# Performance work log

Measured on AMD Instinct MI355X. Metric: run time of the kernel, lower is better.

Reference implementation:

```python
import jax, jax.numpy as jnp
import numpy as np

LAYER_SIZE = [784, 128, 64, 10]
ACTIVE_FUN = ["relu", "relu", "linear"]
BATCH = 65536


def setup_inputs() -> dict:
    key = jax.random.key(0)
    k_x, k0, k1, k2 = jax.random.split(key, 4)
    X = jax.random.normal(k_x, (BATCH, LAYER_SIZE[0]), dtype=jnp.float32)
    # weights mimic torch init: 0.1 * rand(in+1, out)
    W0 = 0.1 * jax.random.uniform(k0, (LAYER_SIZE[0] + 1, LAYER_SIZE[1]), dtype=jnp.float32)
    W1 = 0.1 * jax.random.uniform(k1, (LAYER_SIZE[1] + 1, LAYER_SIZE[2]), dtype=jnp.float32)
    W2 = 0.1 * jax.random.uniform(k2, (LAYER_SIZE[2] + 1, LAYER_SIZE[3]), dtype=jnp.float32)
    return {"X": X, "W0": W0, "W1": W1, "W2": W2}


def _act(h, name):
    if name == "sigmoid":
        return jax.nn.sigmoid(h)
    if name == "relu":
        return jnp.maximum(h, 0.0)
    if name == "tanh":
        return jnp.tanh(h)
    return h  # linear


def _mlp(X, weights):
    h = X
    for W, act in zip(weights, ACTIVE_FUN):
        # bias folded in: concat a column of ones (original concats scalar 1 per sample)
        ones = jnp.ones((h.shape[0], 1), dtype=h.dtype)
        h = jnp.concatenate([h, ones], axis=1) @ W
        h = _act(h, act)
    return h


def reference(X, W0, W1, W2):
    # Batched equivalent of the per-sample Python loop: returns [B, 10] predictions
    return _mlp(X, [W0, W1, W2])
```

## Files before the change

kernel.cpp:

```cpp
#include <hip/hip_runtime.h>

typedef unsigned short u16;
typedef __attribute__((ext_vector_type(4))) float f32x4;
typedef __attribute__((ext_vector_type(8))) short short8;

#define D0 784
#define D1 128
#define D2 64
#define D3 10
#define KS0 25
#define KS1 4
#define KS2 2

#define WS_W0P 0
#define WS_W1P 204800
#define WS_W2P 221184
#define WS_B0  223232
#define WS_B1  223744
#define WS_B2  224000

__device__ __forceinline__ u16 f2bf(float f) {
  union { float f; unsigned u; } v; v.f = f;
  unsigned u = v.u;
  return (u16)((u + 0x7fffu + ((u >> 16) & 1u)) >> 16);
}

__device__ __forceinline__ int swz(int c, int kk) {
  return c * 32 + (((kk >> 3) ^ ((c >> 1) & 3)) << 3) + (kk & 7);
}

__global__ void prep_kernel(const float* __restrict__ W0, const float* __restrict__ W1,
                            const float* __restrict__ W2, u16* __restrict__ w0p,
                            u16* __restrict__ w1p, u16* __restrict__ w2p,
                            float* __restrict__ b0, float* __restrict__ b1,
                            float* __restrict__ b2) {
  int idx = blockIdx.x * 256 + threadIdx.x;
  if (idx < 25 * 128 * 32) {
    int ks = idx / 4096, rem = idx % 4096, c = rem >> 5, kk = rem & 31;
    int k = ks * 32 + kk;
    float v = (k < D0) ? W0[k * D1 + c] : 0.f;
    w0p[ks * 4096 + swz(c, kk)] = f2bf(v);
    return;
  }
  idx -= 25 * 128 * 32;
  if (idx < 4 * 64 * 32) {
    int ks = idx / 2048, rem = idx % 2048, c = rem >> 5, kk = rem & 31;
    int k = ks * 32 + kk;
    w1p[ks * 2048 + swz(c, kk)] = f2bf(W1[k * D2 + c]);
    return;
  }
  idx -= 4 * 64 * 32;
  if (idx < 2 * 16 * 32) {
    int ks = idx / 512, rem = idx % 512, c = rem >> 5, kk = rem & 31;
    int k = ks * 32 + kk;
    float v = (c < D3) ? W2[k * D3 + c] : 0.f;
    w2p[ks * 512 + swz(c, kk)] = f2bf(v);
    return;
  }
  idx -= 2 * 16 * 32;
  if (idx < 128) { b0[idx] = W0[D0 * D1 + idx]; return; }
  idx -= 128;
  if (idx < 64) { b1[idx] = W1[D1 * D2 + idx]; return; }
  idx -= 64;
  if (idx < 16) { b2[idx] = (idx < D3) ? W2[D2 * D3 + idx] : 0.f; }
}

__device__ __forceinline__ void gload_lds16(const void* g, void* l) {
  __builtin_amdgcn_global_load_lds((const __attribute__((address_space(1))) void*)g,
                                   (__attribute__((address_space(3))) void*)l, 16, 0, 0);
}

__device__ __forceinline__ void cvtpk(unsigned& d, float lo, float hi) {
  asm("v_cvt_pk_bf16_f32 %0, %1, %2" : "=v"(d) : "v"(lo), "v"(hi));
}

__global__ __launch_bounds__(256, 4) void mlp_fused(
    const float* __restrict__ X, const u16* __restrict__ w0p,
    const u16* __restrict__ w1p, const float* __restrict__ b0,
    const float* __restrict__ b1, const float* __restrict__ b2,
    float* __restrict__ out) {
  __shared__ __attribute__((aligned(16))) u16 smW0[2][4096];
  __shared__ __attribute__((aligned(16))) u16 smW12[9216];

  const int t = threadIdx.x;
  const int lane = t & 63;
  const int wv = t >> 6;
  const int q = lane >> 4;
  const int lr = lane & 15;

  {
    const char* src = (const char*)w1p;
    char* dst = (char*)smW12;
    for (int off = wv * 1024; off < 18432; off += 4096)
      gload_lds16(src + off + lane * 16, dst + off);
  }
  auto stageW0 = [&](int buf, int ks) {
    const char* src = (const char*)(w0p + ks * 4096) + wv * 2048 + lane * 16;
    char* dst = (char*)&smW0[buf][0] + wv * 2048;
    gload_lds16(src, dst);
    gload_lds16(src + 1024, dst + 1024);
  };

  const int row = blockIdx.x * 64 + wv * 16 + lr;
  const float* xrow = X + (size_t)row * D0;

  f32x4 acc0[8];
#pragma unroll
  for (int f = 0; f < 8; ++f) acc0[f] = (f32x4){0.f, 0.f, 0.f, 0.f};

  f32x4 xa, xb;
  {
    const f32x4* xp = (const f32x4*)(xrow + q * 8);
    xa = xp[0]; xb = xp[1];
  }
  stageW0(0, 0);
  __syncthreads();

  const int boff = lr * 32 + (q ^ ((lr >> 1) & 3)) * 8;

  int buf = 0;
  for (int ks = 0; ks < KS0; ++ks) {
    if (ks + 1 < KS0) stageW0(buf ^ 1, ks + 1);
    f32x4 na = (f32x4){0.f, 0.f, 0.f, 0.f}, nb = (f32x4){0.f, 0.f, 0.f, 0.f};
    if (ks + 1 < KS0) {
      int kb = (ks + 1) * 32 + q * 8;
      if (kb < D0) {
        const f32x4* xp = (const f32x4*)(xrow + kb);
        na = xp[0]; nb = xp[1];
      }
    }
    union { short8 s; unsigned u[4]; } a;
    cvtpk(a.u[0], xa[0], xa[1]);
    cvtpk(a.u[1], xa[2], xa[3]);
    cvtpk(a.u[2], xb[0], xb[1]);
    cvtpk(a.u[3], xb[2], xb[3]);
    const u16* smb = &smW0[buf][0];
#pragma unroll
    for (int f = 0; f < 8; ++f) {
      short8 b = *(const short8*)(smb + f * 512 + boff);
      acc0[f] = __builtin_amdgcn_mfma_f32_16x16x32_bf16(a.s, b, acc0[f], 0, 0, 0);
    }
    __syncthreads();
    xa = na; xb = nb; buf ^= 1;
  }

  char* hbase = (char*)&smW0[0][0] + wv * 4096;

#pragma unroll
  for (int f = 0; f < 8; ++f) {
    int c = f * 16 + lr;
    float bb = b0[c];
    int chb = ((c >> 3) << 4);
    int cwb = (c & 7) << 1;
#pragma unroll
    for (int r = 0; r < 4; ++r) {
      int rr = q * 4 + r;
      float v = acc0[f][r] + bb;
      *(u16*)(hbase + rr * 256 + (chb ^ ((rr & 7) << 4)) + cwb) = f2bf(fmaxf(v, 0.f));
    }
  }
  __builtin_amdgcn_wave_barrier();

  f32x4 acc1[4];
#pragma unroll
  for (int f = 0; f < 4; ++f) acc1[f] = (f32x4){0.f, 0.f, 0.f, 0.f};
#pragma unroll
  for (int ks = 0; ks < KS1; ++ks) {
    short8 a = *(const short8*)(hbase + lr * 256 + (((ks * 4 + q) ^ (lr & 7)) << 4));
#pragma unroll
    for (int f = 0; f < 4; ++f) {
      int c = f * 16 + lr;
      int js = q ^ ((c >> 1) & 3);
      short8 b = *(const short8*)(smW12 + ks * 2048 + c * 32 + js * 8);
      acc1[f] = __builtin_amdgcn_mfma_f32_16x16x32_bf16(a, b, acc1[f], 0, 0, 0);
    }
  }
#pragma unroll
  for (int f = 0; f < 4; ++f) {
    int c = f * 16 + lr;
    float bb = b1[c];
    int chb = ((c >> 3) << 4);
    int cwb = (c & 7) << 1;
#pragma unroll
    for (int r = 0; r < 4; ++r) {
      int rr = q * 4 + r;
      *(u16*)(hbase + rr * 128 + (chb ^ ((rr & 7) << 4)) + cwb) =
          f2bf(fmaxf(acc1[f][r] + bb, 0.f));
    }
  }
  __builtin_amdgcn_wave_barrier();

  f32x4 acc2 = (f32x4){0.f, 0.f, 0.f, 0.f};
  const u16* w2sm = smW12 + 8192;
#pragma unroll
  for (int ks = 0; ks < KS2; ++ks) {
    short8 a = *(const short8*)(hbase + lr * 128 + (((ks * 4 + q) ^ (lr & 7)) << 4));
    int js = q ^ ((lr >> 1) & 3);
    short8 b = *(const short8*)(w2sm + ks * 512 + lr * 32 + js * 8);
    acc2 = __builtin_amdgcn_mfma_f32_16x16x32_bf16(a, b, acc2, 0, 0, 0);
  }
  if (lr < D3) {
    float bb = b2[lr];
#pragma unroll
    for (int r = 0; r < 4; ++r) {
      int rowg = blockIdx.x * 64 + wv * 16 + q * 4 + r;
      out[rowg * D3 + lr] = acc2[r] + bb;
    }
  }
}

extern "C" void kernel_launch(void* const* d_in, const int* in_sizes, int n_in,
                              void* d_out, int out_size, void* d_ws, size_t ws_size,
                              hipStream_t stream) {
  const float* X  = (const float*)d_in[0];
  const float* W0 = (const float*)d_in[1];
  const float* W1 = (const float*)d_in[2];
  const float* W2 = (const float*)d_in[3];
  float* out = (float*)d_out;
  char* ws = (char*)d_ws;
  u16* w0p = (u16*)(ws + WS_W0P);
  u16* w1p = (u16*)(ws + WS_W1P);
  u16* w2p = (u16*)(ws + WS_W2P);
  float* b0 = (float*)(ws + WS_B0);
  float* b1 = (float*)(ws + WS_B1);
  float* b2 = (float*)(ws + WS_B2);

  prep_kernel<<<437, 256, 0, stream>>>(W0, W1, W2, w0p, w1p, w2p, b0, b1, b2);
  mlp_fused<<<65536 / 64, 256, 0, stream>>>(X, w0p, w1p, b0, b1, b2, out);
}
```

Measured before the change: 45.22 us.

## Read weights directly from global/L2 and process two row tiles per wave

```diff
diff --git a/kernel.cpp b/kernel.cpp
--- a/kernel.cpp
+++ b/kernel.cpp
@@ -23,10 +23,6 @@
   union { float f; unsigned u; } v; v.f = f;
   unsigned u = v.u;
   return (u16)((u + 0x7fffu + ((u >> 16) & 1u)) >> 16);
-}
-
-__device__ __forceinline__ int swz(int c, int kk) {
-  return c * 32 + (((kk >> 3) ^ ((c >> 1) & 3)) << 3) + (kk & 7);
 }
 
 __global__ void prep_kernel(const float* __restrict__ W0, const float* __restrict__ W1,
@@ -39,14 +35,14 @@
     int ks = idx / 4096, rem = idx % 4096, c = rem >> 5, kk = rem & 31;
     int k = ks * 32 + kk;
     float v = (k < D0) ? W0[k * D1 + c] : 0.f;
-    w0p[ks * 4096 + swz(c, kk)] = f2bf(v);
+    w0p[ks * 4096 + c * 32 + kk] = f2bf(v);
     return;
   }
   idx -= 25 * 128 * 32;
   if (idx < 4 * 64 * 32) {
     int ks = idx / 2048, rem = idx % 2048, c = rem >> 5, kk = rem & 31;
     int k = ks * 32 + kk;
-    w1p[ks * 2048 + swz(c, kk)] = f2bf(W1[k * D2 + c]);
+    w1p[ks * 2048 + c * 32 + kk] = f2bf(W1[k * D2 + c]);
     return;
   }
   idx -= 4 * 64 * 32;
@@ -54,7 +50,7 @@
     int ks = idx / 512, rem = idx % 512, c = rem >> 5, kk = rem & 31;
     int k = ks * 32 + kk;
     float v = (c < D3) ? W2[k * D3 + c] : 0.f;
-    w2p[ks * 512 + swz(c, kk)] = f2bf(v);
+    w2p[ks * 512 + c * 32 + kk] = f2bf(v);
     return;
   }
   idx -= 2 * 16 * 32;
@@ -65,22 +61,16 @@
   if (idx < 16) { b2[idx] = (idx < D3) ? W2[D2 * D3 + idx] : 0.f; }
 }
 
-__device__ __forceinline__ void gload_lds16(const void* g, void* l) {
-  __builtin_amdgcn_global_load_lds((const __attribute__((address_space(1))) void*)g,
-                                   (__attribute__((address_space(3))) void*)l, 16, 0, 0);
-}
-
 __device__ __forceinline__ void cvtpk(unsigned& d, float lo, float hi) {
   asm("v_cvt_pk_bf16_f32 %0, %1, %2" : "=v"(d) : "v"(lo), "v"(hi));
 }
 
-__global__ __launch_bounds__(256, 4) void mlp_fused(
+__global__ __launch_bounds__(256, 2) void mlp_fused(
     const float* __restrict__ X, const u16* __restrict__ w0p,
-    const u16* __restrict__ w1p, const float* __restrict__ b0,
-    const float* __restrict__ b1, const float* __restrict__ b2,
-    float* __restrict__ out) {
-  __shared__ __attribute__((aligned(16))) u16 smW0[2][4096];
-  __shared__ __attribute__((aligned(16))) u16 smW12[9216];
+    const u16* __restrict__ w1p, const u16* __restrict__ w2p,
+    const float* __restrict__ b0, const float* __restrict__ b1,
+    const float* __restrict__ b2, float* __restrict__ out) {
+  __shared__ __attribute__((aligned(16))) u16 smH[4][4096];
 
   const int t = threadIdx.x;
   const int lane = t & 63;
@@ -88,124 +78,139 @@
   const int q = lane >> 4;
   const int lr = lane & 15;
 
+  const int rowbase = blockIdx.x * 128 + wv * 32;
+  const float* xr0 = X + (size_t)(rowbase + lr) * D0;
+  const float* xr1 = xr0 + (size_t)16 * D0;
+  const u16* bp0 = w0p + lr * 32 + q * 8;
+
+  f32x4 acc[2][8];
+#pragma unroll
+  for (int m = 0; m < 2; ++m)
+#pragma unroll
+    for (int f = 0; f < 8; ++f) acc[m][f] = (f32x4){0.f, 0.f, 0.f, 0.f};
+
+#pragma unroll
+  for (int ks = 0; ks < KS0 - 1; ++ks) {
+    const f32x4* xp0 = (const f32x4*)(xr0 + ks * 32 + q * 8);
+    const f32x4* xp1 = (const f32x4*)(xr1 + ks * 32 + q * 8);
+    f32x4 x0a = xp0[0], x0b = xp0[1];
+    f32x4 x1a = xp1[0], x1b = xp1[1];
+    short8 b[8];
+#pragma unroll
+    for (int f = 0; f < 8; ++f)
+      b[f] = *(const short8*)(bp0 + ks * 4096 + f * 512);
+    union { short8 s; unsigned u[4]; } a0, a1;
+    cvtpk(a0.u[0], x0a[0], x0a[1]); cvtpk(a0.u[1], x0a[2], x0a[3]);
+    cvtpk(a0.u[2], x0b[0], x0b[1]); cvtpk(a0.u[3], x0b[2], x0b[3]);
+    cvtpk(a1.u[0], x1a[0], x1a[1]); cvtpk(a1.u[1], x1a[2], x1a[3]);
+    cvtpk(a1.u[2], x1b[0], x1b[1]); cvtpk(a1.u[3], x1b[2], x1b[3]);
+#pragma unroll
+    for (int f = 0; f < 8; ++f) {
+      acc[0][f] = __builtin_amdgcn_mfma_f32_16x16x32_bf16(a0.s, b[f], acc[0][f], 0, 0, 0);
+      acc[1][f] = __builtin_amdgcn_mfma_f32_16x16x32_bf16(a1.s, b[f], acc[1][f], 0, 0, 0);
+    }
+  }
   {
-    const char* src = (const char*)w1p;
-    char* dst = (char*)smW12;
-    for (int off = wv * 1024; off < 18432; off += 4096)
-      gload_lds16(src + off + lane * 16, dst + off);
-  }
-  auto stageW0 = [&](int buf, int ks) {
-    const char* src = (const char*)(w0p + ks * 4096) + wv * 2048 + lane * 16;
-    char* dst = (char*)&smW0[buf][0] + wv * 2048;
-    gload_lds16(src, dst);
-    gload_lds16(src + 1024, dst + 1024);
-  };
-
-  const int row = blockIdx.x * 64 + wv * 16 + lr;
-  const float* xrow = X + (size_t)row * D0;
-
-  f32x4 acc0[8];
-#pragma unroll
-  for (int f = 0; f < 8; ++f) acc0[f] = (f32x4){0.f, 0.f, 0.f, 0.f};
-
-  f32x4 xa, xb;
-  {
-    const f32x4* xp = (const f32x4*)(xrow + q * 8);
-    xa = xp[0]; xb = xp[1];
-  }
-  stageW0(0, 0);
-  __syncthreads();
-
-  const int boff = lr * 32 + (q ^ ((lr >> 1) & 3)) * 8;
-
-  int buf = 0;
-  for (int ks = 0; ks < KS0; ++ks) {
-    if (ks + 1 < KS0) stageW0(buf ^ 1, ks + 1);
-    f32x4 na = (f32x4){0.f, 0.f, 0.f, 0.f}, nb = (f32x4){0.f, 0.f, 0.f, 0.f};
-    if (ks + 1 < KS0) {
-      int kb = (ks + 1) * 32 + q * 8;
-      if (kb < D0) {
-        const f32x4* xp = (const f32x4*)(xrow + kb);
-        na = xp[0]; nb = xp[1];
-      }
-    }
-    union { short8 s; unsigned u[4]; } a;
-    cvtpk(a.u[0], xa[0], xa[1]);
-    cvtpk(a.u[1], xa[2], xa[3]);
-    cvtpk(a.u[2], xb[0], xb[1]);
-    cvtpk(a.u[3], xb[2], xb[3]);
-    const u16* smb = &smW0[buf][0];
+    const int ks = KS0 - 1;
+    f32x4 x0a = (f32x4){0.f, 0.f, 0.f, 0.f}, x0b = x0a, x1a = x0a, x1b = x0a;
+    if (q < 2) {
+      const f32x4* xp0 = (const f32x4*)(xr0 + ks * 32 + q * 8);
+      const f32x4* xp1 = (const f32x4*)(xr1 + ks * 32 + q * 8);
+      x0a = xp0[0]; x0b = xp0[1];
+      x1a = xp1[0]; x1b = xp1[1];
+    }
+    short8 b[8];
+#pragma unroll
+    for (int f = 0; f < 8; ++f)
+      b[f] = *(const short8*)(bp0 + ks * 4096 + f * 512);
+    union { short8 s; unsigned u[4]; } a0, a1;
+    cvtpk(a0.u[0], x0a[0], x0a[1]); cvtpk(a0.u[1], x0a[2], x0a[3]);
+    cvtpk(a0.u[2], x0b[0], x0b[1]); cvtpk(a0.u[3], x0b[2], x0b[3]);
+    cvtpk(a1.u[0], x1a[0], x1a[1]); cvtpk(a1.u[1], x1a[2], x1a[3]);
+    cvtpk(a1.u[2], x1b[0], x1b[1]); cvtpk(a1.u[3], x1b[2], x1b[3]);
 #pragma unroll
     for (int f = 0; f < 8; ++f) {
-      short8 b = *(const short8*)(smb + f * 512 + boff);
-      acc0[f] = __builtin_amdgcn_mfma_f32_16x16x32_bf16(a.s, b, acc0[f], 0, 0, 0);
-    }
-    __syncthreads();
-    xa = na; xb = nb; buf ^= 1;
-  }
-
-  char* hbase = (char*)&smW0[0][0] + wv * 4096;
-
+      acc[0][f] = __builtin_amdgcn_mfma_f32_16x16x32_bf16(a0.s, b[f], acc[0][f], 0, 0, 0);
+      acc[1][f] = __builtin_amdgcn_mfma_f32_16x16x32_bf16(a1.s, b[f], acc[1][f], 0, 0, 0);
+    }
+  }
+
+  char* hbase = (char*)&smH[wv][0];
 #pragma unroll
   for (int f = 0; f < 8; ++f) {
     int c = f * 16 + lr;
     float bb = b0[c];
-    int chb = ((c >> 3) << 4);
+    int chb = (c >> 3) << 4;
     int cwb = (c & 7) << 1;
 #pragma unroll
-    for (int r = 0; r < 4; ++r) {
-      int rr = q * 4 + r;
-      float v = acc0[f][r] + bb;
-      *(u16*)(hbase + rr * 256 + (chb ^ ((rr & 7) << 4)) + cwb) = f2bf(fmaxf(v, 0.f));
-    }
+    for (int m = 0; m < 2; ++m)
+#pragma unroll
+      for (int r = 0; r < 4; ++r) {
+        int rr = m * 16 + q * 4 + r;
+        *(u16*)(hbase + rr * 256 + (chb ^ ((rr & 7) << 4)) + cwb) =
+            f2bf(fmaxf(acc[m][f][r] + bb, 0.f));
+      }
   }
   __builtin_amdgcn_wave_barrier();
 
-  f32x4 acc1[4];
-#pragma unroll
-  for (int f = 0; f < 4; ++f) acc1[f] = (f32x4){0.f, 0.f, 0.f, 0.f};
+  f32x4 acc1[2][4];
+#pragma unroll
+  for (int m = 0; m < 2; ++m)
+#pragma unroll
+    for (int f = 0; f < 4; ++f) acc1[m][f] = (f32x4){0.f, 0.f, 0.f, 0.f};
+  const u16* bp1 = w1p + lr * 32 + q * 8;
 #pragma unroll
   for (int ks = 0; ks < KS1; ++ks) {
-    short8 a = *(const short8*)(hbase + lr * 256 + (((ks * 4 + q) ^ (lr & 7)) << 4));
+    short8 a0 = *(const short8*)(hbase + lr * 256 + (((ks * 4 + q) ^ (lr & 7)) << 4));
+    short8 a1 = *(const short8*)(hbase + (16 + lr) * 256 + (((ks * 4 + q) ^ (lr & 7)) << 4));
+    short8 b[4];
+#pragma unroll
+    for (int f = 0; f < 4; ++f)
+      b[f] = *(const short8*)(bp1 + ks * 2048 + f * 512);
 #pragma unroll
     for (int f = 0; f < 4; ++f) {
-      int c = f * 16 + lr;
-      int js = q ^ ((c >> 1) & 3);
-      short8 b = *(const short8*)(smW12 + ks * 2048 + c * 32 + js * 8);
-      acc1[f] = __builtin_amdgcn_mfma_f32_16x16x32_bf16(a, b, acc1[f], 0, 0, 0);
+      acc1[0][f] = __builtin_amdgcn_mfma_f32_16x16x32_bf16(a0, b[f], acc1[0][f], 0, 0, 0);
+      acc1[1][f] = __builtin_amdgcn_mfma_f32_16x16x32_bf16(a1, b[f], acc1[1][f], 0, 0, 0);
     }
   }
 #pragma unroll
   for (int f = 0; f < 4; ++f) {
     int c = f * 16 + lr;
     float bb = b1[c];
-    int chb = ((c >> 3) << 4);
+    int chb = (c >> 3) << 4;
     int cwb = (c & 7) << 1;
 #pragma unroll
-    for (int r = 0; r < 4; ++r) {
-      int rr = q * 4 + r;
-      *(u16*)(hbase + rr * 128 + (chb ^ ((rr & 7) << 4)) + cwb) =
-          f2bf(fmaxf(acc1[f][r] + bb, 0.f));
-    }
+    for (int m = 0; m < 2; ++m)
+#pragma unroll
+      for (int r = 0; r < 4; ++r) {
+        int rr = m * 16 + q * 4 + r;
+        *(u16*)(hbase + rr * 128 + (chb ^ ((rr & 7) << 4)) + cwb) =
+            f2bf(fmaxf(acc1[m][f][r] + bb, 0.f));
+      }
   }
   __builtin_amdgcn_wave_barrier();
 
-  f32x4 acc2 = (f32x4){0.f, 0.f, 0.f, 0.f};
-  const u16* w2sm = smW12 + 8192;
+  f32x4 acc2[2];
+  acc2[0] = (f32x4){0.f, 0.f, 0.f, 0.f};
+  acc2[1] = (f32x4){0.f, 0.f, 0.f, 0.f};
+  const u16* bp2 = w2p + lr * 32 + q * 8;
 #pragma unroll
   for (int ks = 0; ks < KS2; ++ks) {
-    short8 a = *(const short8*)(hbase + lr * 128 + (((ks * 4 + q) ^ (lr & 7)) << 4));
-    int js = q ^ ((lr >> 1) & 3);
-    short8 b = *(const short8*)(w2sm + ks * 512 + lr * 32 + js * 8);
-    acc2 = __builtin_amdgcn_mfma_f32_16x16x32_bf16(a, b, acc2, 0, 0, 0);
+    short8 a0 = *(const short8*)(hbase + lr * 128 + (((ks * 4 + q) ^ (lr & 7)) << 4));
+    short8 a1 = *(const short8*)(hbase + (16 + lr) * 128 + (((ks * 4 + q) ^ (lr & 7)) << 4));
+    short8 b = *(const short8*)(bp2 + ks * 512);
+    acc2[0] = __builtin_amdgcn_mfma_f32_16x16x32_bf16(a0, b, acc2[0], 0, 0, 0);
+    acc2[1] = __builtin_amdgcn_mfma_f32_16x16x32_bf16(a1, b, acc2[1], 0, 0, 0);
   }
   if (lr < D3) {
     float bb = b2[lr];
 #pragma unroll
-    for (int r = 0; r < 4; ++r) {
-      int rowg = blockIdx.x * 64 + wv * 16 + q * 4 + r;
-      out[rowg * D3 + lr] = acc2[r] + bb;
-    }
+    for (int m = 0; m < 2; ++m)
+#pragma unroll
+      for (int r = 0; r < 4; ++r) {
+        int rowg = rowbase + m * 16 + q * 4 + r;
+        out[rowg * D3 + lr] = acc2[m][r] + bb;
+      }
   }
 }
 
@@ -226,5 +231,5 @@
   float* b2 = (float*)(ws + WS_B2);
 
   prep_kernel<<<437, 256, 0, stream>>>(W0, W1, W2, w0p, w1p, w2p, b0, b1, b2);
-  mlp_fused<<<65536 / 64, 256, 0, stream>>>(X, w0p, w1p, b0, b1, b2, out);
-}
+  mlp_fused<<<65536 / 128, 256, 0, stream>>>(X, w0p, w1p, w2p, b0, b1, b2, out);
+}
```

Measured after the change: 57.66 us. 27.5% more time.

## Halve block size to two waves and read layer-1/2 weights from global

Applied to the files above, without the earlier changes.

```diff
diff --git a/kernel.cpp b/kernel.cpp
--- a/kernel.cpp
+++ b/kernel.cpp
@@ -35,18 +35,18 @@
                             float* __restrict__ b0, float* __restrict__ b1,
                             float* __restrict__ b2) {
   int idx = blockIdx.x * 256 + threadIdx.x;
-  if (idx < 25 * 128 * 32) {
+  if (idx < KS0 * 4096) {
     int ks = idx / 4096, rem = idx % 4096, c = rem >> 5, kk = rem & 31;
     int k = ks * 32 + kk;
     float v = (k < D0) ? W0[k * D1 + c] : 0.f;
     w0p[ks * 4096 + swz(c, kk)] = f2bf(v);
     return;
   }
-  idx -= 25 * 128 * 32;
+  idx -= KS0 * 4096;
   if (idx < 4 * 64 * 32) {
     int ks = idx / 2048, rem = idx % 2048, c = rem >> 5, kk = rem & 31;
     int k = ks * 32 + kk;
-    w1p[ks * 2048 + swz(c, kk)] = f2bf(W1[k * D2 + c]);
+    w1p[ks * 2048 + c * 32 + kk] = f2bf(W1[k * D2 + c]);
     return;
   }
   idx -= 4 * 64 * 32;
@@ -54,7 +54,7 @@
     int ks = idx / 512, rem = idx % 512, c = rem >> 5, kk = rem & 31;
     int k = ks * 32 + kk;
     float v = (c < D3) ? W2[k * D3 + c] : 0.f;
-    w2p[ks * 512 + swz(c, kk)] = f2bf(v);
+    w2p[ks * 512 + c * 32 + kk] = f2bf(v);
     return;
   }
   idx -= 2 * 16 * 32;
@@ -74,13 +74,12 @@
   asm("v_cvt_pk_bf16_f32 %0, %1, %2" : "=v"(d) : "v"(lo), "v"(hi));
 }
 
-__global__ __launch_bounds__(256, 4) void mlp_fused(
+__global__ __launch_bounds__(128, 4) void mlp_fused(
     const float* __restrict__ X, const u16* __restrict__ w0p,
-    const u16* __restrict__ w1p, const float* __restrict__ b0,
-    const float* __restrict__ b1, const float* __restrict__ b2,
-    float* __restrict__ out) {
+    const u16* __restrict__ w1p, const u16* __restrict__ w2p,
+    const float* __restrict__ b0, const float* __restrict__ b1,
+    const float* __restrict__ b2, float* __restrict__ out) {
   __shared__ __attribute__((aligned(16))) u16 smW0[2][4096];
-  __shared__ __attribute__((aligned(16))) u16 smW12[9216];
 
   const int t = threadIdx.x;
   const int lane = t & 63;
@@ -88,25 +87,21 @@
   const int q = lane >> 4;
   const int lr = lane & 15;
 
-  {
-    const char* src = (const char*)w1p;
-    char* dst = (char*)smW12;
-    for (int off = wv * 1024; off < 18432; off += 4096)
-      gload_lds16(src + off + lane * 16, dst + off);
-  }
+  const int rowbase = blockIdx.x * 32 + wv * 16;
+  const float* xrow = X + (size_t)(rowbase + lr) * D0;
+
   auto stageW0 = [&](int buf, int ks) {
-    const char* src = (const char*)(w0p + ks * 4096) + wv * 2048 + lane * 16;
-    char* dst = (char*)&smW0[buf][0] + wv * 2048;
+    const char* src = (const char*)(w0p + ks * 4096) + wv * 4096 + lane * 16;
+    char* dst = (char*)&smW0[buf][0] + wv * 4096;
     gload_lds16(src, dst);
     gload_lds16(src + 1024, dst + 1024);
+    gload_lds16(src + 2048, dst + 2048);
+    gload_lds16(src + 3072, dst + 3072);
   };
 
-  const int row = blockIdx.x * 64 + wv * 16 + lr;
-  const float* xrow = X + (size_t)row * D0;
-
-  f32x4 acc0[8];
-#pragma unroll
-  for (int f = 0; f < 8; ++f) acc0[f] = (f32x4){0.f, 0.f, 0.f, 0.f};
+  f32x4 acc[8];
+#pragma unroll
+  for (int f = 0; f < 8; ++f) acc[f] = (f32x4){0.f, 0.f, 0.f, 0.f};
 
   f32x4 xa, xb;
   {
@@ -120,7 +115,6 @@
 
   int buf = 0;
   for (int ks = 0; ks < KS0; ++ks) {
-    if (ks + 1 < KS0) stageW0(buf ^ 1, ks + 1);
     f32x4 na = (f32x4){0.f, 0.f, 0.f, 0.f}, nb = (f32x4){0.f, 0.f, 0.f, 0.f};
     if (ks + 1 < KS0) {
       int kb = (ks + 1) * 32 + q * 8;
@@ -128,6 +122,7 @@
         const f32x4* xp = (const f32x4*)(xrow + kb);
         na = xp[0]; nb = xp[1];
       }
+      stageW0(buf ^ 1, ks + 1);
     }
     union { short8 s; unsigned u[4]; } a;
     cvtpk(a.u[0], xa[0], xa[1]);
@@ -138,7 +133,7 @@
 #pragma unroll
     for (int f = 0; f < 8; ++f) {
       short8 b = *(const short8*)(smb + f * 512 + boff);
-      acc0[f] = __builtin_amdgcn_mfma_f32_16x16x32_bf16(a.s, b, acc0[f], 0, 0, 0);
+      acc[f] = __builtin_amdgcn_mfma_f32_16x16x32_bf16(a.s, b, acc[f], 0, 0, 0);
     }
     __syncthreads();
     xa = na; xb = nb; buf ^= 1;
@@ -150,13 +145,13 @@
   for (int f = 0; f < 8; ++f) {
     int c = f * 16 + lr;
     float bb = b0[c];
-    int chb = ((c >> 3) << 4);
+    int chb = (c >> 3) << 4;
     int cwb = (c & 7) << 1;
 #pragma unroll
     for (int r = 0; r < 4; ++r) {
       int rr = q * 4 + r;
-      float v = acc0[f][r] + bb;
-      *(u16*)(hbase + rr * 256 + (chb ^ ((rr & 7) << 4)) + cwb) = f2bf(fmaxf(v, 0.f));
+      *(u16*)(hbase + rr * 256 + (chb ^ ((rr & 7) << 4)) + cwb) =
+          f2bf(fmaxf(acc[f][r] + bb, 0.f));
     }
   }
   __builtin_amdgcn_wave_barrier();
@@ -164,22 +159,23 @@
   f32x4 acc1[4];
 #pragma unroll
   for (int f = 0; f < 4; ++f) acc1[f] = (f32x4){0.f, 0.f, 0.f, 0.f};
+  const u16* bp1 = w1p + lr * 32 + q * 8;
 #pragma unroll
   for (int ks = 0; ks < KS1; ++ks) {
     short8 a = *(const short8*)(hbase + lr * 256 + (((ks * 4 + q) ^ (lr & 7)) << 4));
-#pragma unroll
-    for (int f = 0; f < 4; ++f) {
-      int c = f * 16 + lr;
-      int js = q ^ ((c >> 1) & 3);
-      short8 b = *(const short8*)(smW12 + ks * 2048 + c * 32 + js * 8);
-      acc1[f] = __builtin_amdgcn_mfma_f32_16x16x32_bf16(a, b, acc1[f], 0, 0, 0);
-    }
+    short8 b[4];
+#pragma unroll
+    for (int f = 0; f < 4; ++f)
+      b[f] = *(const short8*)(bp1 + ks * 2048 + f * 512);
+#pragma unroll
+    for (int f = 0; f < 4; ++f)
+      acc1[f] = __builtin_amdgcn_mfma_f32_16x16x32_bf16(a, b[f], acc1[f], 0, 0, 0);
   }
 #pragma unroll
   for (int f = 0; f < 4; ++f) {
     int c = f * 16 + lr;
     float bb = b1[c];
-    int chb = ((c >> 3) << 4);
+    int chb = (c >> 3) << 4;
     int cwb = (c & 7) << 1;
 #pragma unroll
     for (int r = 0; r < 4; ++r) {
@@ -191,19 +187,18 @@
   __builtin_amdgcn_wave_barrier();
 
   f32x4 acc2 = (f32x4){0.f, 0.f, 0.f, 0.f};
-  const u16* w2sm = smW12 + 8192;
+  const u16* bp2 = w2p + lr * 32 + q * 8;
 #pragma unroll
   for (int ks = 0; ks < KS2; ++ks) {
     short8 a = *(const short8*)(hbase + lr * 128 + (((ks * 4 + q) ^ (lr & 7)) << 4));
-    int js = q ^ ((lr >> 1) & 3);
-    short8 b = *(const short8*)(w2sm + ks * 512 + lr * 32 + js * 8);
+    short8 b = *(const short8*)(bp2 + ks * 512);
     acc2 = __builtin_amdgcn_mfma_f32_16x16x32_bf16(a, b, acc2, 0, 0, 0);
   }
   if (lr < D3) {
     float bb = b2[lr];
 #pragma unroll
     for (int r = 0; r < 4; ++r) {
-      int rowg = blockIdx.x * 64 + wv * 16 + q * 4 + r;
+      int rowg = rowbase + q * 4 + r;
       out[rowg * D3 + lr] = acc2[r] + bb;
     }
   }
@@ -226,5 +221,5 @@
   float* b2 = (float*)(ws + WS_B2);
 
   prep_kernel<<<437, 256, 0, stream>>>(W0, W1, W2, w0p, w1p, w2p, b0, b1, b2);
-  mlp_fused<<<65536 / 64, 256, 0, stream>>>(X, w0p, w1p, b0, b1, b2, out);
-}
+  mlp_fused<<<65536 / 32, 128, 0, stream>>>(X, w0p, w1p, w2p, b0, b1, b2, out);
+}
```

Result: slower. 49.76 us (+10.0%).
